# Kernel tuning notes

Hardware: AMD Instinct MI355X
Metric: run time of the kernel (lower is better)

## Reference

```python
import jax, jax.numpy as jnp
import numpy as np

B, T, F = 2, 128, 88          # batch, time frames, pitch bins (hard-coded 88)
HIDDEN = 64                    # LSTM input dim
N_UNIT = 64                    # channel dim (= 2 * lstm hidden 32)
N_HEAD = 4
HEAD_DIM = N_UNIT // N_HEAD    # 16
WINDOW = 7
N_LAYERS = 2
DIFF_STEPS = 100
LSTM_H = N_UNIT // 2           # 32 per direction


def setup_inputs() -> dict:
    key = jax.random.key(0)
    ks = jax.random.split(key, 12)
    s = 0.05
    inp = {
        'x': jax.random.normal(ks[0], (B, T * F, HIDDEN), jnp.float32),
        't': jax.random.randint(ks[1], (B,), 0, DIFF_STEPS, jnp.int32),
        # LSTM params, stacked [layer, direction, ...]; layer-1 input dim == 2*LSTM_H == HIDDEN
        'lstm_w_ih': s * jax.random.normal(ks[2], (N_LAYERS, 2, 4 * LSTM_H, HIDDEN), jnp.float32),
        'lstm_w_hh': s * jax.random.normal(ks[3], (N_LAYERS, 2, 4 * LSTM_H, LSTM_H), jnp.float32),
        'lstm_b_ih': s * jax.random.normal(ks[4], (N_LAYERS, 2, 4 * LSTM_H), jnp.float32),
        'lstm_b_hh': s * jax.random.normal(ks[5], (N_LAYERS, 2, 4 * LSTM_H), jnp.float32),
        # per-NA-layer params
        't_emb': s * jax.random.normal(ks[6], (N_LAYERS, DIFF_STEPS, N_UNIT), jnp.float32),
        'w_qkv': s * jax.random.normal(ks[7], (N_LAYERS, N_UNIT, 3 * N_UNIT), jnp.float32),
        'b_qkv': jnp.zeros((N_LAYERS, 3 * N_UNIT), jnp.float32),
        'rpb': s * jax.random.normal(ks[8], (N_LAYERS, N_HEAD, 2 * WINDOW - 1, 2 * WINDOW - 1), jnp.float32),
        'w_proj': s * jax.random.normal(ks[9], (N_LAYERS, N_UNIT, N_UNIT), jnp.float32),
        'b_proj': jnp.zeros((N_LAYERS, N_UNIT), jnp.float32),
    }
    return inp


def _lstm_dir(x, w_ih, w_hh, b_ih, b_hh, reverse):
    # x: [N, T, D]; pytorch gate order i, f, g, o
    N = x.shape[0]
    H = w_hh.shape[1]
    xs = jnp.swapaxes(x, 0, 1)
    if reverse:
        xs = xs[::-1]
    b = b_ih + b_hh
    def step(carry, xt):
        h, c = carry
        g = xt @ w_ih.T + h @ w_hh.T + b
        i, f, gg, o = jnp.split(g, 4, axis=-1)
        c = jax.nn.sigmoid(f) * c + jax.nn.sigmoid(i) * jnp.tanh(gg)
        h = jax.nn.sigmoid(o) * jnp.tanh(c)
        return (h, c), h
    h0 = jnp.zeros((N, H), x.dtype)
    _, hs = jax.lax.scan(step, (h0, h0), xs)
    if reverse:
        hs = hs[::-1]
    return jnp.swapaxes(hs, 0, 1)


def _bilstm(x, w_ih, w_hh, b_ih, b_hh):
    for l in range(w_ih.shape[0]):
        fwd = _lstm_dir(x, w_ih[l, 0], w_hh[l, 0], b_ih[l, 0], b_hh[l, 0], False)
        bwd = _lstm_dir(x, w_ih[l, 1], w_hh[l, 1], b_ih[l, 1], b_hh[l, 1], True)
        x = jnp.concatenate([fwd, bwd], axis=-1)
    return x


def _nbh(L, w):
    # NATTEN-style clamped (non-shrinking) neighborhood window per axis
    i = jnp.arange(L)
    start = jnp.clip(i - w // 2, 0, L - w)
    idx = start[:, None] + jnp.arange(w)[None, :]   # [L, w] absolute neighbor idx
    rel = idx - i[:, None] + (w - 1)                # [L, w] rel-pos-bias idx in [0, 2w-2]
    return idx, rel


def _na2d(x, t_idx, emb, wqkv, bqkv, rpb_l, wproj, bproj):
    # x: [B, Th, Tw, C]; diffusion-step conditioning via learned embedding add
    Bx, Th, Tw, C = x.shape
    h = x + emb[t_idx][:, None, None, :]
    qkv = (h @ wqkv + bqkv).reshape(Bx, Th, Tw, 3, N_HEAD, HEAD_DIM)
    q = jnp.moveaxis(qkv[..., 0, :, :], 3, 1) * (HEAD_DIM ** -0.5)  # [B,h,Th,Tw,d]
    k = jnp.moveaxis(qkv[..., 1, :, :], 3, 1)
    v = jnp.moveaxis(qkv[..., 2, :, :], 3, 1)
    ih, rh = _nbh(Th, WINDOW)
    iw, rw = _nbh(Tw, WINDOW)
    # gather windowed neighbors: [B,h,Th,Tw,w,w,d]
    kn = k[:, :, ih[:, None, :, None], iw[None, :, None, :], :]
    vn = v[:, :, ih[:, None, :, None], iw[None, :, None, :], :]
    bias = rpb_l[:, rh[:, None, :, None], rw[None, :, None, :]]     # [h,Th,Tw,w,w]
    logits = jnp.einsum('bhijd,bhijkld->bhijkl', q, kn) + bias[None]
    attn = jax.nn.softmax(logits.reshape(Bx, N_HEAD, Th, Tw, -1), axis=-1).reshape(logits.shape)
    out = jnp.einsum('bhijkl,bhijkld->bhijd', attn, vn)             # [B,h,Th,Tw,d]
    out = jnp.moveaxis(out, 1, 3).reshape(Bx, Th, Tw, C)
    return out @ wproj + bproj


def reference(x, t, lstm_w_ih, lstm_w_hh, lstm_b_ih, lstm_b_hh,
              t_emb, w_qkv, b_qkv, rpb, w_proj, b_proj):
    Bx = x.shape[0]
    Hin = x.shape[-1]
    Tt = x.shape[1] // F
    h = x.reshape(Bx, Tt, F, Hin).transpose(0, 2, 1, 3).reshape(Bx * F, Tt, Hin)
    h = _bilstm(h, lstm_w_ih, lstm_w_hh, lstm_b_ih, lstm_b_hh)      # [B*88, T, n_unit]
    # -> [B, T, 88, n_unit] 2D grid (height=T, width=88)
    h = h.reshape(Bx, F, Tt, N_UNIT).transpose(0, 2, 1, 3)
    for l in range(N_LAYERS):
        h = h + _na2d(h, t, t_emb[l], w_qkv[l], b_qkv[l], rpb[l], w_proj[l], b_proj[l])
    return h
```

## Files before the change

### kernel.cpp

```cpp
#include <hip/hip_runtime.h>
#include <math.h>

#define B_ 2
#define T_ 128
#define F_ 88
#define HID 64
#define NU 64
#define NH 4
#define HD 16
#define LH 32
#define NSEQ (B_*F_)
#define NTOK (B_*T_*F_)
#define NPOS (T_*F_)

__device__ __forceinline__ float fsig(float x) {
    return __builtin_amdgcn_rcpf(1.0f + __expf(-x));
}
__device__ __forceinline__ float ftanh(float x) {
    return 2.0f * __builtin_amdgcn_rcpf(1.0f + __expf(-2.0f*x)) - 1.0f;
}

template<int LAYER>
__global__ void __launch_bounds__(256, 2) gg_kernel(
    const float* __restrict__ xin,
    const float* __restrict__ w_ih,
    const float* __restrict__ b_ih,
    const float* __restrict__ b_hh,
    float* __restrict__ G)
{
    __shared__ __align__(16) float xts[32][68];
    __shared__ __align__(16) float wsh[256][68];
    __shared__ float bsh[256];
    const int s  = blockIdx.x;
    const int t0 = blockIdx.y * 32;
    const int b = s / F_, f = s % F_;
    const int tid = threadIdx.x;

    for (int n = tid; n < 32*64; n += 256) {
        const int tt = n >> 6, k = n & 63;
        xts[tt][k] = (LAYER == 0)
            ? xin[(((size_t)b*T_ + t0+tt)*F_ + f)*HID + k]
            : xin[((size_t)s*T_ + t0+tt)*HID + k];
    }
    for (int n = tid; n < 256*64; n += 256) {
        const int row = n >> 6, k = n & 63;
        wsh[row][k] = w_ih[((size_t)LAYER*256 + row)*HID + k];
    }
    bsh[tid] = b_ih[LAYER*256 + tid] + b_hh[LAYER*256 + tid];
    __syncthreads();

    const int lane = tid & 63;
    const int g    = tid >> 6;
    const int dir  = g >> 1;
    const int th   = g & 1;
    const int rowA = dir*128 + lane;
    const int rowB = dir*128 + 64 + lane;

    float accA[16] = {}, accB[16] = {};
    #pragma unroll 4
    for (int k4 = 0; k4 < 16; k4++) {
        const float4 wA = *(const float4*)&wsh[rowA][k4*4];
        const float4 wB = *(const float4*)&wsh[rowB][k4*4];
        #pragma unroll
        for (int tt = 0; tt < 16; tt++) {
            const float4 xv = *(const float4*)&xts[th*16+tt][k4*4];
            accA[tt] += wA.x*xv.x + wA.y*xv.y + wA.z*xv.z + wA.w*xv.w;
            accB[tt] += wB.x*xv.x + wB.y*xv.y + wB.z*xv.z + wB.w*xv.w;
        }
    }
    const float bA = bsh[rowA], bB = bsh[rowB];
    float* gbase = G + (((size_t)(s*2+dir)*T_ + t0 + th*16)*LH + (lane & 31))*4
                     + (lane >> 5)*2;
    #pragma unroll
    for (int tt = 0; tt < 16; tt++) {
        float2 o; o.x = accA[tt] + bA; o.y = accB[tt] + bB;
        *(float2*)(gbase + (size_t)tt*128) = o;
    }
}

template<int LAYER>
__global__ void __launch_bounds__(64, 1) lstm_rec(
    const float* __restrict__ G,
    const float* __restrict__ w_hh,
    float* __restrict__ outp)
{
    __shared__ float hbuf[2][T_][LH];
    const int p   = blockIdx.x;
    const int dir = p & 1;
    const int sA  = (p >> 1) * 2;
    const int sB  = sA + 1;
    const int lane = threadIdx.x;
    const int u    = lane & 31;
    const int half = lane >> 5;
    const int s    = half ? sB : sA;
    const int b = s / F_, f = s % F_;

    float wi[LH], wf[LH], wg[LH], wo[LH];
    {
        const float* wb = w_hh + (size_t)((LAYER*2+dir)*128)*LH;
        const float4* pi = (const float4*)(wb + (size_t)(0*LH + u)*LH);
        const float4* pf = (const float4*)(wb + (size_t)(1*LH + u)*LH);
        const float4* pg = (const float4*)(wb + (size_t)(2*LH + u)*LH);
        const float4* po = (const float4*)(wb + (size_t)(3*LH + u)*LH);
        #pragma unroll
        for (int k4 = 0; k4 < LH/4; k4++) {
            float4 a = pi[k4], bq = pf[k4], cq = pg[k4], dq = po[k4];
            wi[k4*4+0]=a.x;  wi[k4*4+1]=a.y;  wi[k4*4+2]=a.z;  wi[k4*4+3]=a.w;
            wf[k4*4+0]=bq.x; wf[k4*4+1]=bq.y; wf[k4*4+2]=bq.z; wf[k4*4+3]=bq.w;
            wg[k4*4+0]=cq.x; wg[k4*4+1]=cq.y; wg[k4*4+2]=cq.z; wg[k4*4+3]=cq.w;
            wo[k4*4+0]=dq.x; wo[k4*4+1]=dq.y; wo[k4*4+2]=dq.z; wo[k4*4+3]=dq.w;
        }
    }
    const int chain = s*2 + dir;
    const float4* gp = (const float4*)G + (size_t)chain*T_*LH + u;
    #define GTIME(st) (dir ? (T_-1-(st)) : (st))

    float h = 0.f, c = 0.f;

    #define STEP(g4, stepi)                                                  \
    {                                                                        \
        float ci = (g4).x, cg = (g4).y, cf = (g4).z, co = (g4).w;            \
        float ci1 = 0.f, cg1 = 0.f, cf1 = 0.f, co1 = 0.f;                    \
        _Pragma("unroll")                                                    \
        for (int k = 0; k < 16; k++) {                                       \
            const float hk  = __shfl(h, k, 32);          \
            const float hk2 = __shfl(h, k+16, 32);                           \
            ci  += wi[k]*hk;     cg  += wg[k]*hk;                            \
            cf  += wf[k]*hk;     co  += wo[k]*hk;                            \
            ci1 += wi[k+16]*hk2; cg1 += wg[k+16]*hk2;                        \
            cf1 += wf[k+16]*hk2; co1 += wo[k+16]*hk2;                        \
        }                                                                    \
        const float ti = fsig(ci+ci1), tf = fsig(cf+cf1);                    \
        const float to = fsig(co+co1), tg = ftanh(cg+cg1);                   \
        c = tf*c + ti*tg;                                                    \
        h = to * ftanh(c);                                                   \
        hbuf[half][GTIME(stepi)][u] = h;                                     \
    }

    float4 A[4], Bf[4];
    #pragma unroll
    for (int i = 0; i < 4; i++) A[i]  = gp[(size_t)GTIME(i)*LH];
    #pragma unroll
    for (int i = 0; i < 4; i++) Bf[i] = gp[(size_t)GTIME(4+i)*LH];

    #pragma unroll 1
    for (int grp = 0; grp < 32; grp++) {
        float4 P[4];
        const int pf4 = (grp < 30 ? grp + 2 : 31) * 4;
        #pragma unroll
        for (int i = 0; i < 4; i++) P[i] = gp[(size_t)GTIME(pf4+i)*LH];
        #pragma unroll
        for (int i = 0; i < 4; i++) { STEP(A[i], grp*4 + i); }
        #pragma unroll
        for (int i = 0; i < 4; i++) { A[i] = Bf[i]; Bf[i] = P[i]; }
    }
    #undef STEP
    #undef GTIME
    __syncthreads();

    const float4* l4 = (const float4*)&hbuf[half][0][0];
    if (LAYER == 0) {
        for (int idx = u; idx < T_*8; idx += 32) {
            const int t = idx >> 3, q = idx & 7;
            *(float4*)&outp[((size_t)s*T_ + t)*NU + dir*LH + q*4] = l4[idx];
        }
    } else {
        for (int idx = u; idx < T_*8; idx += 32) {
            const int t = idx >> 3, q = idx & 7;
            *(float4*)&outp[(((size_t)b*T_ + t)*F_ + f)*NU + dir*LH + q*4] = l4[idx];
        }
    }
}

__global__ void __launch_bounds__(256, 2) qkv_kernel(
    const float* __restrict__ hcur,
    const int*   __restrict__ tarr,
    const float* __restrict__ t_emb,
    const float* __restrict__ w_qkv,
    const float* __restrict__ b_qkv,
    const int layer,
    float* __restrict__ qb, float* __restrict__ kb, float* __restrict__ vb)
{
    __shared__ float as[64][65];
    __shared__ float wsh[64][64];
    const int m0 = blockIdx.x * 64;
    const int which = blockIdx.y;
    const int tid = threadIdx.x;
    const int bidx = m0 / NPOS;
    const int tb = tarr[bidx];
    const float* embp = t_emb + ((size_t)layer*100 + tb)*HID;

    for (int n = tid; n < 64*64; n += 256) {
        const int mm = n >> 6, k = n & 63;
        as[mm][k]  = hcur[((size_t)m0+mm)*64 + k] + embp[k];
        wsh[mm][k] = w_qkv[((size_t)layer*64 + mm)*192 + which*64 + k];
    }
    __syncthreads();

    const int tm = tid >> 4, tn = tid & 15;
    float acc[4][4] = {};
    for (int k = 0; k < 64; k++) {
        const float a0 = as[tm*4+0][k];
        const float a1 = as[tm*4+1][k];
        const float a2 = as[tm*4+2][k];
        const float a3 = as[tm*4+3][k];
        const float4 w = *(const float4*)&wsh[k][tn*4];
        acc[0][0]+=a0*w.x; acc[0][1]+=a0*w.y; acc[0][2]+=a0*w.z; acc[0][3]+=a0*w.w;
        acc[1][0]+=a1*w.x; acc[1][1]+=a1*w.y; acc[1][2]+=a1*w.z; acc[1][3]+=a1*w.w;
        acc[2][0]+=a2*w.x; acc[2][1]+=a2*w.y; acc[2][2]+=a2*w.z; acc[2][3]+=a2*w.w;
        acc[3][0]+=a3*w.x; acc[3][1]+=a3*w.y; acc[3][2]+=a3*w.z; acc[3][3]+=a3*w.w;
    }

    float* dst = (which == 0) ? qb : (which == 1) ? kb : vb;
    const float scale = (which == 0) ? 0.25f : 1.0f;
    const int hh = tn >> 2;
    const int dbase = (tn & 3) * 4;
    const float4 bv = *(const float4*)&b_qkv[(size_t)layer*192 + which*64 + tn*4];
    #pragma unroll
    for (int r = 0; r < 4; r++) {
        const int row = m0 + tm*4 + r;
        const int pos = row - bidx*NPOS;
        float4 o;
        o.x = (acc[r][0] + bv.x) * scale;
        o.y = (acc[r][1] + bv.y) * scale;
        o.z = (acc[r][2] + bv.z) * scale;
        o.w = (acc[r][3] + bv.w) * scale;
        *(float4*)&dst[(((size_t)bidx*NH + hh)*NPOS + pos)*HD + dbase] = o;
    }
}

__global__ void __launch_bounds__(192, 1) nattn_kernel(
    const float* __restrict__ qb,
    const float* __restrict__ kb,
    const float* __restrict__ vb,
    const float* __restrict__ rpb,
    const int layer,
    float* __restrict__ ao)
{
    __shared__ float ks[8][88][20];
    __shared__ float rp[169];
    const int blk = blockIdx.x;
    const int bh = blk & 7;
    const int it = blk >> 3;
    const int i0 = it*2;
    const int h  = bh & 3;
    const int bb = bh >> 2;
    const int tid = threadIdx.x;
    const int rs = min(max(i0-3, 0), T_-8);
    const float* kbase = kb + (size_t)bh*NPOS*HD;
    const float* vbase = vb + (size_t)bh*NPOS*HD;

    const bool act = (tid < 2*F_);
    const int isub = act ? (tid / F_) : 0;
    const int j    = act ? (tid - isub*F_) : 0;
    const int i    = i0 + isub;
    const int ihs  = min(max(i-3, 0), T_-7);
    const int ro   = ihs - rs;
    const int cw   = min(max(j-3, 0), F_-7);

    float4 q0, q1, q2, q3;
    if (act) {
        const float4* qp = (const float4*)&qb[((size_t)bh*NPOS + i*F_ + j)*HD];
        q0 = qp[0]; q1 = qp[1]; q2 = qp[2]; q3 = qp[3];
    }
    for (int n = tid; n < 169; n += 192)
        rp[n] = rpb[((size_t)layer*NH + h)*169 + n];
    for (int n4 = tid; n4 < 8*88*4; n4 += 192) {
        const int d4   = n4 & 3;
        const int rest = n4 >> 2;
        const int c    = rest % 88;
        const int r    = rest / 88;
        *(float4*)&ks[r][c][d4*4] =
            *(const float4*)&kbase[((size_t)(rs+r)*F_ + c)*HD + d4*4];
    }
    __syncthreads();

    float lg[49];
    if (act) {
        #pragma unroll
        for (int ki = 0; ki < 7; ki++) {
            const int rh = ihs + ki - i + 6;
            #pragma unroll
            for (int kj = 0; kj < 7; kj++) {
                const float4* kp = (const float4*)&ks[ro+ki][cw+kj][0];
                const float4 k0 = kp[0], k1 = kp[1], k2 = kp[2], k3 = kp[3];
                float d = q0.x*k0.x + q0.y*k0.y + q0.z*k0.z + q0.w*k0.w
                        + q1.x*k1.x + q1.y*k1.y + q1.z*k1.z + q1.w*k1.w
                        + q2.x*k2.x + q2.y*k2.y + q2.z*k2.z + q2.w*k2.w
                        + q3.x*k3.x + q3.y*k3.y + q3.z*k3.z + q3.w*k3.w;
                lg[ki*7+kj] = d + rp[rh*13 + (cw + kj - j + 6)];
            }
        }
        float m = lg[0];
        #pragma unroll
        for (int n = 1; n < 49; n++) m = fmaxf(m, lg[n]);
        float ssum = 0.f;
        #pragma unroll
        for (int n = 0; n < 49; n++) { lg[n] = __expf(lg[n] - m); ssum += lg[n]; }
        const float inv = __builtin_amdgcn_rcpf(ssum);
        #pragma unroll
        for (int n = 0; n < 49; n++) lg[n] *= inv;
    }
    __syncthreads();
    for (int n4 = tid; n4 < 8*88*4; n4 += 192) {
        const int d4   = n4 & 3;
        const int rest = n4 >> 2;
        const int c    = rest % 88;
        const int r    = rest / 88;
        *(float4*)&ks[r][c][d4*4] =
            *(const float4*)&vbase[((size_t)(rs+r)*F_ + c)*HD + d4*4];
    }
    __syncthreads();
    if (act) {
        float4 o0 = {0,0,0,0}, o1 = {0,0,0,0}, o2 = {0,0,0,0}, o3 = {0,0,0,0};
        #pragma unroll
        for (int ki = 0; ki < 7; ki++) {
            #pragma unroll
            for (int kj = 0; kj < 7; kj++) {
                const float a = lg[ki*7+kj];
                const float4* vp = (const float4*)&ks[ro+ki][cw+kj][0];
                const float4 v0 = vp[0], v1 = vp[1], v2 = vp[2], v3 = vp[3];
                o0.x += a*v0.x; o0.y += a*v0.y; o0.z += a*v0.z; o0.w += a*v0.w;
                o1.x += a*v1.x; o1.y += a*v1.y; o1.z += a*v1.z; o1.w += a*v1.w;
                o2.x += a*v2.x; o2.y += a*v2.y; o2.z += a*v2.z; o2.w += a*v2.w;
                o3.x += a*v3.x; o3.y += a*v3.y; o3.z += a*v3.z; o3.w += a*v3.w;
            }
        }
        float4* op = (float4*)&ao[(((size_t)bb*T_ + i)*F_ + j)*NU + h*HD];
        op[0]=o0; op[1]=o1; op[2]=o2; op[3]=o3;
    }
}

__global__ void __launch_bounds__(256, 2) proj_kernel(
    const float* __restrict__ ain,
    const float* __restrict__ hres,
    const float* __restrict__ w_proj,
    const float* __restrict__ b_proj,
    const int layer,
    float* __restrict__ outp)
{
    __shared__ float as[64][65];
    __shared__ float wsh[64][64];
    const int m0 = blockIdx.x * 64;
    const int tid = threadIdx.x;
    for (int n = tid; n < 64*64; n += 256) {
        const int mm = n >> 6, k = n & 63;
        as[mm][k]  = ain[((size_t)m0+mm)*64 + k];
        wsh[mm][k] = w_proj[(size_t)layer*4096 + n];
    }
    __syncthreads();
    const int tm = tid >> 4, tn = tid & 15;
    float acc[4][4] = {};
    for (int k = 0; k < 64; k++) {
        const float a0 = as[tm*4+0][k];
        const float a1 = as[tm*4+1][k];
        const float a2 = as[tm*4+2][k];
        const float a3 = as[tm*4+3][k];
        const float4 w = *(const float4*)&wsh[k][tn*4];
        acc[0][0]+=a0*w.x; acc[0][1]+=a0*w.y; acc[0][2]+=a0*w.z; acc[0][3]+=a0*w.w;
        acc[1][0]+=a1*w.x; acc[1][1]+=a1*w.y; acc[1][2]+=a1*w.z; acc[1][3]+=a1*w.w;
        acc[2][0]+=a2*w.x; acc[2][1]+=a2*w.y; acc[2][2]+=a2*w.z; acc[2][3]+=a2*w.w;
        acc[3][0]+=a3*w.x; acc[3][1]+=a3*w.y; acc[3][2]+=a3*w.z; acc[3][3]+=a3*w.w;
    }
    const float4 bv = *(const float4*)&b_proj[(size_t)layer*64 + tn*4];
    #pragma unroll
    for (int r = 0; r < 4; r++) {
        const int row = m0 + tm*4 + r;
        const float4 hv = *(const float4*)&hres[(size_t)row*64 + tn*4];
        float4 o;
        o.x = hv.x + acc[r][0] + bv.x;
        o.y = hv.y + acc[r][1] + bv.y;
        o.z = hv.z + acc[r][2] + bv.z;
        o.w = hv.w + acc[r][3] + bv.w;
        *(float4*)&outp[(size_t)row*64 + tn*4] = o;
    }
}

extern "C" void kernel_launch(void* const* d_in, const int* in_sizes, int n_in,
                              void* d_out, int out_size, void* d_ws, size_t ws_size,
                              hipStream_t stream) {
    const float* x      = (const float*)d_in[0];
    const int*   tarr   = (const int*)  d_in[1];
    const float* w_ih   = (const float*)d_in[2];
    const float* w_hh   = (const float*)d_in[3];
    const float* b_ih   = (const float*)d_in[4];
    const float* b_hh   = (const float*)d_in[5];
    const float* t_emb  = (const float*)d_in[6];
    const float* w_qkv  = (const float*)d_in[7];
    const float* b_qkv  = (const float*)d_in[8];
    const float* rpb    = (const float*)d_in[9];
    const float* w_proj = (const float*)d_in[10];
    const float* b_proj = (const float*)d_in[11];

    float* ws   = (float*)d_ws;
    const size_t CH = (size_t)NTOK * NU;
    float* hcur = ws;
    float* h0   = ws + CH;
    float* G    = ws + 2*CH;
    float* qbuf = ws + 2*CH;
    float* kbuf = ws + 3*CH;
    float* vbuf = ws + 4*CH;
    float* ao   = ws + 5*CH;
    float* outp = (float*)d_out;

    gg_kernel<0><<<dim3(NSEQ, T_/32), 256, 0, stream>>>(x,  w_ih, b_ih, b_hh, G);
    lstm_rec<0><<<NSEQ, 64, 0, stream>>>(G, w_hh, h0);
    gg_kernel<1><<<dim3(NSEQ, T_/32), 256, 0, stream>>>(h0, w_ih, b_ih, b_hh, G);
    lstm_rec<1><<<NSEQ, 64, 0, stream>>>(G, w_hh, hcur);

    for (int l = 0; l < 2; l++) {
        qkv_kernel<<<dim3(NTOK/64, 3), 256, 0, stream>>>(
            hcur, tarr, t_emb, w_qkv, b_qkv, l, qbuf, kbuf, vbuf);
        nattn_kernel<<<(T_/2)*8, 192, 0, stream>>>(
            qbuf, kbuf, vbuf, rpb, l, ao);
        proj_kernel<<<NTOK/64, 256, 0, stream>>>(
            ao, hcur, w_proj, b_proj, l, (l == 0) ? hcur : outp);
    }
}
```

Baseline: 277.8 us.

## Broadcast LSTM hidden state through LDS and merge K/V staging in neighborhood attention

The recurrent LSTM kernel now gives each block one sequence, with its two directions in the two halves of the wave. The hidden state is broadcast through a small LDS staging buffer read as float4, replacing 32 cross-lane shuffles per step. Output rows are written as full 64-wide float4 rows. The neighborhood attention kernel now handles 4 query rows per 384-thread block and loads K and V tiles into LDS together, removing one barrier and the second load phase. This costs more LDS per block and halves the number of blocks.

```diff
diff --git a/kernel.cpp b/kernel.cpp
--- a/kernel.cpp
+++ b/kernel.cpp
@@ -84,16 +84,13 @@
     const float* __restrict__ w_hh,
     float* __restrict__ outp)
 {
-    __shared__ float hbuf[2][T_][LH];
-    const int p   = blockIdx.x;
-    const int dir = p & 1;
-    const int sA  = (p >> 1) * 2;
-    const int sB  = sA + 1;
+    __shared__ float hbuf[T_][NU];
+    __shared__ __align__(16) float hstage[2][LH];
+    const int s = blockIdx.x;
+    const int b = s / F_, f = s % F_;
     const int lane = threadIdx.x;
     const int u    = lane & 31;
-    const int half = lane >> 5;
-    const int s    = half ? sB : sA;
-    const int b = s / F_, f = s % F_;
+    const int dir  = lane >> 5;
 
     float wi[LH], wf[LH], wg[LH], wo[LH];
     {
@@ -111,30 +108,36 @@
             wo[k4*4+0]=dq.x; wo[k4*4+1]=dq.y; wo[k4*4+2]=dq.z; wo[k4*4+3]=dq.w;
         }
     }
-    const int chain = s*2 + dir;
-    const float4* gp = (const float4*)G + (size_t)chain*T_*LH + u;
+    const float4* gp = (const float4*)G + (size_t)(s*2+dir)*T_*LH + u;
     #define GTIME(st) (dir ? (T_-1-(st)) : (st))
 
     float h = 0.f, c = 0.f;
+    hstage[dir][u] = 0.f;
 
     #define STEP(g4, stepi)                                                  \
     {                                                                        \
-        float ci = (g4).x, cg = (g4).y, cf = (g4).z, co = (g4).w;            \
-        float ci1 = 0.f, cg1 = 0.f, cf1 = 0.f, co1 = 0.f;                    \
+        float hbc[LH];                                                       \
+        _Pragma("unroll")                                                    \
+        for (int q = 0; q < 8; q++) {                                        \
+            const float4 hv = *(const float4*)&hstage[dir][q*4];             \
+            hbc[q*4+0]=hv.x; hbc[q*4+1]=hv.y;                                \
+            hbc[q*4+2]=hv.z; hbc[q*4+3]=hv.w;                                \
+        }                                                                    \
+        float ci0=(g4).x, cg0=(g4).y, cf0=(g4).z, co0=(g4).w;                \
+        float ci1=0.f, cg1=0.f, cf1=0.f, co1=0.f;                            \
         _Pragma("unroll")                                                    \
         for (int k = 0; k < 16; k++) {                                       \
-            const float hk  = __shfl(h, k, 32);          \
-            const float hk2 = __shfl(h, k+16, 32);                           \
-            ci  += wi[k]*hk;     cg  += wg[k]*hk;                            \
-            cf  += wf[k]*hk;     co  += wo[k]*hk;                            \
-            ci1 += wi[k+16]*hk2; cg1 += wg[k+16]*hk2;                        \
-            cf1 += wf[k+16]*hk2; co1 += wo[k+16]*hk2;                        \
+            ci0 += wi[k]*hbc[k];       cg0 += wg[k]*hbc[k];                  \
+            cf0 += wf[k]*hbc[k];       co0 += wo[k]*hbc[k];                  \
+            ci1 += wi[k+16]*hbc[k+16]; cg1 += wg[k+16]*hbc[k+16];            \
+            cf1 += wf[k+16]*hbc[k+16]; co1 += wo[k+16]*hbc[k+16];            \
         }                                                                    \
-        const float ti = fsig(ci+ci1), tf = fsig(cf+cf1);                    \
-        const float to = fsig(co+co1), tg = ftanh(cg+cg1);                   \
+        const float ti = fsig(ci0+ci1), tf = fsig(cf0+cf1);                  \
+        const float to = fsig(co0+co1), tg = ftanh(cg0+cg1);                 \
         c = tf*c + ti*tg;                                                    \
         h = to * ftanh(c);                                                   \
-        hbuf[half][GTIME(stepi)][u] = h;                                     \
+        hbuf[GTIME(stepi)][dir*LH + u] = h;                                  \
+        hstage[dir][u] = h;                                                  \
     }
 
     float4 A[4], Bf[4];
@@ -158,16 +161,15 @@
     #undef GTIME
     __syncthreads();
 
-    const float4* l4 = (const float4*)&hbuf[half][0][0];
+    const float4* lds4 = (const float4*)&hbuf[0][0];
     if (LAYER == 0) {
-        for (int idx = u; idx < T_*8; idx += 32) {
-            const int t = idx >> 3, q = idx & 7;
-            *(float4*)&outp[((size_t)s*T_ + t)*NU + dir*LH + q*4] = l4[idx];
-        }
+        float4* out4 = (float4*)outp + (size_t)s*T_*16;
+        for (int idx = lane; idx < T_*16; idx += 64)
+            out4[idx] = lds4[idx];
     } else {
-        for (int idx = u; idx < T_*8; idx += 32) {
-            const int t = idx >> 3, q = idx & 7;
-            *(float4*)&outp[(((size_t)b*T_ + t)*F_ + f)*NU + dir*LH + q*4] = l4[idx];
+        for (int idx = lane; idx < T_*16; idx += 64) {
+            const int t = idx >> 4, c4 = idx & 15;
+            ((float4*)outp)[(((size_t)b*T_ + t)*F_ + f)*16 + c4] = lds4[idx];
         }
     }
 }
@@ -229,7 +231,7 @@
     }
 }
 
-__global__ void __launch_bounds__(192, 1) nattn_kernel(
+__global__ void __launch_bounds__(384, 1) nattn_kernel(
     const float* __restrict__ qb,
     const float* __restrict__ kb,
     const float* __restrict__ vb,
@@ -237,20 +239,20 @@
     const int layer,
     float* __restrict__ ao)
 {
-    __shared__ float ks[8][88][20];
+    __shared__ float kv[2][10][88][20];
     __shared__ float rp[169];
     const int blk = blockIdx.x;
     const int bh = blk & 7;
     const int it = blk >> 3;
-    const int i0 = it*2;
+    const int i0 = it*4;
     const int h  = bh & 3;
     const int bb = bh >> 2;
     const int tid = threadIdx.x;
-    const int rs = min(max(i0-3, 0), T_-8);
+    const int rs = min(max(i0-3, 0), T_-10);
     const float* kbase = kb + (size_t)bh*NPOS*HD;
     const float* vbase = vb + (size_t)bh*NPOS*HD;
 
-    const bool act = (tid < 2*F_);
+    const bool act = (tid < 4*F_);
     const int isub = act ? (tid / F_) : 0;
     const int j    = act ? (tid - isub*F_) : 0;
     const int i    = i0 + isub;
@@ -263,26 +265,27 @@
         const float4* qp = (const float4*)&qb[((size_t)bh*NPOS + i*F_ + j)*HD];
         q0 = qp[0]; q1 = qp[1]; q2 = qp[2]; q3 = qp[3];
     }
-    for (int n = tid; n < 169; n += 192)
+    for (int n = tid; n < 169; n += 384)
         rp[n] = rpb[((size_t)layer*NH + h)*169 + n];
-    for (int n4 = tid; n4 < 8*88*4; n4 += 192) {
+    for (int n4 = tid; n4 < 10*88*4; n4 += 384) {
         const int d4   = n4 & 3;
         const int rest = n4 >> 2;
         const int c    = rest % 88;
         const int r    = rest / 88;
-        *(float4*)&ks[r][c][d4*4] =
-            *(const float4*)&kbase[((size_t)(rs+r)*F_ + c)*HD + d4*4];
+        const size_t goff = ((size_t)(rs+r)*F_ + c)*HD + d4*4;
+        *(float4*)&kv[0][r][c][d4*4] = *(const float4*)&kbase[goff];
+        *(float4*)&kv[1][r][c][d4*4] = *(const float4*)&vbase[goff];
     }
     __syncthreads();
 
-    float lg[49];
     if (act) {
+        float lg[49];
         #pragma unroll
         for (int ki = 0; ki < 7; ki++) {
             const int rh = ihs + ki - i + 6;
             #pragma unroll
             for (int kj = 0; kj < 7; kj++) {
-                const float4* kp = (const float4*)&ks[ro+ki][cw+kj][0];
+                const float4* kp = (const float4*)&kv[0][ro+ki][cw+kj][0];
                 const float4 k0 = kp[0], k1 = kp[1], k2 = kp[2], k3 = kp[3];
                 float d = q0.x*k0.x + q0.y*k0.y + q0.z*k0.z + q0.w*k0.w
                         + q1.x*k1.x + q1.y*k1.y + q1.z*k1.z + q1.w*k1.w
@@ -300,25 +303,14 @@
         const float inv = __builtin_amdgcn_rcpf(ssum);
         #pragma unroll
         for (int n = 0; n < 49; n++) lg[n] *= inv;
-    }
-    __syncthreads();
-    for (int n4 = tid; n4 < 8*88*4; n4 += 192) {
-        const int d4   = n4 & 3;
-        const int rest = n4 >> 2;
-        const int c    = rest % 88;
-        const int r    = rest / 88;
-        *(float4*)&ks[r][c][d4*4] =
-            *(const float4*)&vbase[((size_t)(rs+r)*F_ + c)*HD + d4*4];
-    }
-    __syncthreads();
-    if (act) {
+
         float4 o0 = {0,0,0,0}, o1 = {0,0,0,0}, o2 = {0,0,0,0}, o3 = {0,0,0,0};
         #pragma unroll
         for (int ki = 0; ki < 7; ki++) {
             #pragma unroll
             for (int kj = 0; kj < 7; kj++) {
                 const float a = lg[ki*7+kj];
-                const float4* vp = (const float4*)&ks[ro+ki][cw+kj][0];
+                const float4* vp = (const float4*)&kv[1][ro+ki][cw+kj][0];
                 const float4 v0 = vp[0], v1 = vp[1], v2 = vp[2], v3 = vp[3];
                 o0.x += a*v0.x; o0.y += a*v0.y; o0.z += a*v0.z; o0.w += a*v0.w;
                 o1.x += a*v1.x; o1.y += a*v1.y; o1.z += a*v1.z; o1.w += a*v1.w;
@@ -411,7 +403,7 @@
     for (int l = 0; l < 2; l++) {
         qkv_kernel<<<dim3(NTOK/64, 3), 256, 0, stream>>>(
             hcur, tarr, t_emb, w_qkv, b_qkv, l, qbuf, kbuf, vbuf);
-        nattn_kernel<<<(T_/2)*8, 192, 0, stream>>>(
+        nattn_kernel<<<(T_/4)*8, 384, 0, stream>>>(
             qbuf, kbuf, vbuf, rpb, l, ao);
         proj_kernel<<<NTOK/64, 256, 0, stream>>>(
             ao, hcur, w_proj, b_proj, l, (l == 0) ? hcur : outp);
```

Result: faster. 251.5 us (-9.4%).
